# Performance work log

Measured on AMD Instinct MI355X. Metric: run time of the kernel, lower is better.

The kernel has to match this reference:

```python
import jax, jax.numpy as jnp
import numpy as np

N, D, B = 50000, 256, 2048
SIGMA = 1.0
SIGMA2 = SIGMA * SIGMA  # module stores np.square(sigma)


def setup_inputs() -> dict:
    key = jax.random.key(0)
    k1, k2, k3, k4 = jax.random.split(key, 4)
    x = jax.random.normal(k1, (B, D), dtype=jnp.float32)
    data_set = jax.random.normal(k2, (N, D), dtype=jnp.float32)
    # labels are +/-1
    data_labels = jnp.where(jax.random.uniform(k3, (N,)) < 0.5, -1.0, 1.0).astype(jnp.float32)
    # lambdas initialized to ones in the module; use small positive noise around 1/n scale
    lambdas = jax.random.uniform(k4, (N,), dtype=jnp.float32) * (2.0 / N)
    b = jnp.ones((1,), dtype=jnp.float32)
    return {"x": x, "data_set": data_set, "data_labels": data_labels,
            "lambdas": lambdas, "b": b}


def reference(x, data_set, data_labels, lambdas, b):
    x2 = jnp.sum(x * x, axis=1, keepdims=True)            # [B,1]
    s2 = jnp.sum(data_set * data_set, axis=1)             # [N]
    cross = jnp.einsum('bd,nd->bn', x, data_set)          # [B,N]
    sqdist = x2 + s2[None, :] - 2.0 * cross               # [B,N]
    K = jnp.exp(-sqdist / (2.0 * SIGMA2))                 # rbf kernel [B,N]
    w = data_labels * jax.nn.relu(lambdas)                # [N]
    return jnp.tanh(K @ w + b)                            # [B]
```

## Files before the change

### kernel.cpp

```cpp
#include <hip/hip_runtime.h>
#include <hip/hip_bf16.h>
#include <math.h>

#define NPTS 50000
#define DIM  256
#define BQ   2048
#define NPAD 50048

#define BK   32
#define CH   64
#define NCH  782
#define NG   48
#define LOG2E 1.4426950408889634f

#define WS_ACC 0
#define WS_X2  2048
#define WS_T   4096
#define WS_SGN 54144
#define WS_XB  104192
#define WS_SB  366336
#define WS_TOTAL_BYTES (6772480ull * 4ull)

#define V1_ACC 0
#define V1_X2  2048
#define V1_S2  4096
#define V1_W   54096

typedef __bf16 bf16x8 __attribute__((ext_vector_type(8)));
typedef __bf16 bf16x4 __attribute__((ext_vector_type(4)));
typedef float  f32x4  __attribute__((ext_vector_type(4)));
typedef unsigned int u32;

__device__ __forceinline__ float fast_exp2(float v) {
#if __has_builtin(__builtin_amdgcn_exp2f)
  return __builtin_amdgcn_exp2f(v);
#else
  return exp2f(v);
#endif
}

__device__ __forceinline__ void async_copy16(const __bf16* g, __bf16* l) {
  __builtin_amdgcn_global_load_lds(
      (const __attribute__((address_space(1))) u32*)g,
      (__attribute__((address_space(3))) u32*)l, 16, 0, 0);
}


__global__ __launch_bounds__(256) void svm_precvt9(
    const float* __restrict__ x, const float* __restrict__ s,
    const float* __restrict__ labels, const float* __restrict__ lambdas,
    float* __restrict__ ws) {
  const int wid  = blockIdx.x * 4 + (threadIdx.x >> 6);
  const int lane = threadIdx.x & 63;
  __bf16* xb = (__bf16*)(ws + WS_XB);
  __bf16* sb = (__bf16*)(ws + WS_SB);

  if (blockIdx.x < 8) ws[WS_ACC + blockIdx.x * 256 + threadIdx.x] = 0.0f;

  if (wid < NPAD) {
    float4 v = make_float4(0.f, 0.f, 0.f, 0.f);
    if (wid < NPTS)
      v = reinterpret_cast<const float4*>(s + (size_t)wid * DIM)[lane];
    bf16x4 h = { (__bf16)v.x, (__bf16)v.y, (__bf16)v.z, (__bf16)v.w };
    *reinterpret_cast<bf16x4*>(sb + (size_t)wid * DIM + lane * 4) = h;
    float ss = v.x * v.x + v.y * v.y + v.z * v.z + v.w * v.w;
    #pragma unroll
    for (int off = 32; off > 0; off >>= 1) ss += __shfl_xor(ss, off);
    if (lane == 0) {
      float s2h = 0.5f * LOG2E * ss;
      float lam = (wid < NPTS) ? lambdas[wid] : 0.0f;
      float lab = (wid < NPTS) ? labels[wid] : 1.0f;
      float mag = lam > 0.0f ? lam : 0.0f;
      ws[WS_T + wid]   = (mag > 0.0f) ? s2h - log2f(mag) : __builtin_inff();
      ws[WS_SGN + wid] = lab;
    }
  } else if (wid < NPAD + BQ) {
    int r = wid - NPAD;
    float4 v = reinterpret_cast<const float4*>(x + (size_t)r * DIM)[lane];
    bf16x4 h = { (__bf16)v.x, (__bf16)v.y, (__bf16)v.z, (__bf16)v.w };
    *reinterpret_cast<bf16x4*>(xb + (size_t)r * DIM + lane * 4) = h;
    float ss = v.x * v.x + v.y * v.y + v.z * v.z + v.w * v.w;
    #pragma unroll
    for (int off = 32; off > 0; off >>= 1) ss += __shfl_xor(ss, off);
    if (lane == 0) ws[WS_X2 + r] = 0.5f * LOG2E * ss;
  }
}

__global__ __launch_bounds__(256, 2) void svm_main9(float* __restrict__ ws) {
  __shared__ __bf16 sB[8 * CH * 32];

  const __bf16* xb = (const __bf16*)(ws + WS_XB);
  const __bf16* sb = (const __bf16*)(ws + WS_SB);
  const float* x2g = ws + WS_X2;
  const float* tg  = ws + WS_T;
  const float* sgg = ws + WS_SGN;
  float* accOut    = ws + WS_ACC;

  const int t    = threadIdx.x;
  const int wave = t >> 6;
  const int lane = t & 63;
  const int quad = lane >> 4;
  const int l16  = lane & 15;
  const int g    = blockIdx.x & 47;
  const int mt   = blockIdx.x / 48;
  const int m0   = mt * 128;
  const int c0   = (NCH * g) / NG;
  const int c1   = (NCH * (g + 1)) / NG;

  f32x4 afr[2][8];
  #pragma unroll
  for (int mi = 0; mi < 2; ++mi)
    #pragma unroll
    for (int kt = 0; kt < 8; ++kt)
      afr[mi][kt] = *reinterpret_cast<const f32x4*>(
          xb + (size_t)(m0 + wave * 32 + mi * 16 + l16) * DIM + kt * BK + quad * 8);
  #pragma unroll
  for (int mi = 0; mi < 2; ++mi)
    #pragma unroll
    for (int kt = 0; kt < 8; ++kt)
      asm volatile("" : "+v"(afr[mi][kt]));

  float runAcc[2][4] = {{0.f, 0.f, 0.f, 0.f}, {0.f, 0.f, 0.f, 0.f}};

  const int srcswz = ((lane & 3) ^ ((lane >> 3) & 3)) * 8;
  const int rdswz = (quad ^ ((l16 >> 1) & 3)) * 8;

  for (int c = c0; c < c1; ++c) {
    __syncthreads();

    #pragma unroll
    for (int i = 0; i < 8; ++i) {
      int ch = wave * 8 + i;
      int kt = ch >> 2;
      int nb = (ch & 3) * 16;
      const __bf16* src = sb + (size_t)(c * CH + nb + (lane >> 2)) * DIM
                             + kt * BK + srcswz;
      async_copy16(src, &sB[kt * (CH * 32) + nb * 32] + lane * 8);
    }
    __syncthreads();

    f32x4 acc[2][4];
    #pragma unroll
    for (int mi = 0; mi < 2; ++mi)
      #pragma unroll
      for (int ni = 0; ni < 4; ++ni)
        acc[mi][ni] = (f32x4)(0.0f);

    #pragma unroll
    for (int kt = 0; kt < 8; ++kt) {
      bf16x8 bfv[4];
      #pragma unroll
      for (int ni = 0; ni < 4; ++ni)
        bfv[ni] = *reinterpret_cast<const bf16x8*>(
            &sB[kt * (CH * 32) + (ni * 16 + l16) * 32 + rdswz]);
      #pragma unroll
      for (int mi = 0; mi < 2; ++mi)
        #pragma unroll
        for (int ni = 0; ni < 4; ++ni)
          acc[mi][ni] = __builtin_amdgcn_mfma_f32_16x16x32_bf16(
              __builtin_bit_cast(bf16x8, afr[mi][kt]), bfv[ni],
              acc[mi][ni], 0, 0, 0);
    }

    float tt[4], sg[4];
    #pragma unroll
    for (int ni = 0; ni < 4; ++ni) {
      int n = c * CH + ni * 16 + l16;
      tt[ni] = tg[n];
      sg[ni] = sgg[n];
    }
    #pragma unroll
    for (int mi = 0; mi < 2; ++mi)
      #pragma unroll
      for (int reg = 0; reg < 4; ++reg) {
        float p = runAcc[mi][reg];
        #pragma unroll
        for (int ni = 0; ni < 4; ++ni)
          p = __builtin_fmaf(sg[ni],
                fast_exp2(__builtin_fmaf(acc[mi][ni][reg], LOG2E, -tt[ni])), p);
        runAcc[mi][reg] = p;
      }
  }

  #pragma unroll
  for (int mi = 0; mi < 2; ++mi)
    #pragma unroll
    for (int reg = 0; reg < 4; ++reg) {
      float v = runAcc[mi][reg];
      v += __shfl_xor(v, 1);
      v += __shfl_xor(v, 2);
      v += __shfl_xor(v, 4);
      v += __shfl_xor(v, 8);
      if (l16 == 0) {
        int row = m0 + wave * 32 + mi * 16 + quad * 4 + reg;
        atomicAdd(&accOut[row], fast_exp2(-x2g[row]) * v);
      }
    }
}


__global__ __launch_bounds__(256) void svm_precompute(
    const float* __restrict__ x, const float* __restrict__ s,
    const float* __restrict__ labels, const float* __restrict__ lambdas,
    float* __restrict__ ws) {
  int wid  = blockIdx.x * 4 + (threadIdx.x >> 6);
  int lane = threadIdx.x & 63;
  const float* src;
  if (wid < NPTS)           src = s + (size_t)wid * DIM;
  else if (wid < NPTS + BQ) src = x + (size_t)(wid - NPTS) * DIM;
  else return;
  float4 v = reinterpret_cast<const float4*>(src)[lane];
  float ss = v.x * v.x + v.y * v.y + v.z * v.z + v.w * v.w;
  #pragma unroll
  for (int off = 32; off > 0; off >>= 1) ss += __shfl_xor(ss, off);
  if (lane == 0) {
    if (wid < NPTS) {
      ws[V1_S2 + wid] = ss;
      float lam = lambdas[wid];
      ws[V1_W + wid] = labels[wid] * (lam > 0.0f ? lam : 0.0f);
    } else {
      ws[V1_X2 + (wid - NPTS)] = ss;
    }
  }
}

__global__ __launch_bounds__(256) void svm_main(
    const float* __restrict__ x, const float* __restrict__ s,
    const float* __restrict__ ws) {
  __shared__ __bf16 sA[128 * BK];
  __shared__ __bf16 sB2[128 * BK];

  const int t    = threadIdx.x;
  const int wave = t >> 6;
  const int lane = t & 63;
  const int quad = lane >> 4;
  const int l16  = lane & 15;
  const int wm   = (wave & 1) * 64;
  const int wn   = (wave >> 1) * 64;
  const int bRow0 = blockIdx.y * 128;
  const int n0    = blockIdx.x * 128;

  f32x4 acc[4][4];
  #pragma unroll
  for (int i = 0; i < 4; ++i)
    #pragma unroll
    for (int j = 0; j < 4; ++j)
      acc[i][j] = (f32x4)(0.0f);

  for (int kt = 0; kt < DIM / BK; ++kt) {
    const int k0 = kt * BK;
    __syncthreads();
    #pragma unroll
    for (int i = 0; i < 4; ++i) {
      int slot = t + i * 256;
      int r  = slot >> 3;
      int c4 = slot & 7;
      float4 va = reinterpret_cast<const float4*>(
          x + (size_t)(bRow0 + r) * DIM + k0)[c4];
      bf16x4 ha = { (__bf16)va.x, (__bf16)va.y, (__bf16)va.z, (__bf16)va.w };
      *reinterpret_cast<bf16x4*>(&sA[r * BK + c4 * 4]) = ha;

      int nrow = n0 + r;
      float4 vb = make_float4(0.f, 0.f, 0.f, 0.f);
      if (nrow < NPTS)
        vb = reinterpret_cast<const float4*>(
            s + (size_t)nrow * DIM + k0)[c4];
      bf16x4 hb = { (__bf16)vb.x, (__bf16)vb.y, (__bf16)vb.z, (__bf16)vb.w };
      *reinterpret_cast<bf16x4*>(&sB2[r * BK + c4 * 4]) = hb;
    }
    __syncthreads();

    bf16x8 af[4], bfv[4];
    #pragma unroll
    for (int mi = 0; mi < 4; ++mi)
      af[mi] = *reinterpret_cast<const bf16x8*>(
          &sA[(wm + mi * 16 + l16) * BK + quad * 8]);
    #pragma unroll
    for (int ni = 0; ni < 4; ++ni)
      bfv[ni] = *reinterpret_cast<const bf16x8*>(
          &sB2[(wn + ni * 16 + l16) * BK + quad * 8]);
    #pragma unroll
    for (int mi = 0; mi < 4; ++mi)
      #pragma unroll
      for (int ni = 0; ni < 4; ++ni)
        acc[mi][ni] = __builtin_amdgcn_mfma_f32_16x16x32_bf16(
            af[mi], bfv[ni], acc[mi][ni], 0, 0, 0);
  }

  const float* x2g = ws + V1_X2;
  const float* s2g = ws + V1_S2;
  const float* wg  = ws + V1_W;
  float* accOut    = (float*)ws + V1_ACC;

  float s2v[4], wv[4];
  #pragma unroll
  for (int ni = 0; ni < 4; ++ni) {
    int n = n0 + wn + ni * 16 + l16;
    bool ok = n < NPTS;
    s2v[ni] = ok ? s2g[n] : 0.0f;
    wv[ni]  = ok ? wg[n]  : 0.0f;
  }
  #pragma unroll
  for (int mi = 0; mi < 4; ++mi) {
    const int mbase = wm + mi * 16 + quad * 4;
    #pragma unroll
    for (int reg = 0; reg < 4; ++reg) {
      float x2r = x2g[bRow0 + mbase + reg];
      float ps = 0.0f;
      #pragma unroll
      for (int ni = 0; ni < 4; ++ni) {
        float cc = acc[mi][ni][reg];
        ps += __expf(__builtin_fmaf(-0.5f, x2r + s2v[ni], cc)) * wv[ni];
      }
      ps += __shfl_xor(ps, 1);
      ps += __shfl_xor(ps, 2);
      ps += __shfl_xor(ps, 4);
      ps += __shfl_xor(ps, 8);
      if (l16 == 0) atomicAdd(&accOut[bRow0 + mbase + reg], ps);
    }
  }
}


__global__ __launch_bounds__(256) void svm_finalize(
    const float* __restrict__ ws, const float* __restrict__ bias,
    float* __restrict__ out) {
  int i = blockIdx.x * 256 + threadIdx.x;
  if (i < BQ) out[i] = tanhf(ws[i] + bias[0]);
}

extern "C" void kernel_launch(void* const* d_in, const int* in_sizes, int n_in,
                              void* d_out, int out_size, void* d_ws, size_t ws_size,
                              hipStream_t stream) {
  const float* x       = (const float*)d_in[0];
  const float* s       = (const float*)d_in[1];
  const float* labels  = (const float*)d_in[2];
  const float* lambdas = (const float*)d_in[3];
  const float* bias    = (const float*)d_in[4];
  float* out = (float*)d_out;
  float* ws  = (float*)d_ws;

  if (ws_size >= WS_TOTAL_BYTES) {
    svm_precvt9<<<(NPAD + BQ + 3) / 4, 256, 0, stream>>>(x, s, labels, lambdas, ws);
    svm_main9<<<16 * NG, 256, 0, stream>>>(ws);
  } else {
    hipMemsetAsync(ws, 0, BQ * sizeof(float), stream);
    svm_precompute<<<(NPTS + BQ + 3) / 4, 256, 0, stream>>>(x, s, labels, lambdas, ws);
    dim3 grid(391, BQ / 128);
    svm_main<<<grid, 256, 0, stream>>>(x, s, ws);
  }
  svm_finalize<<<BQ / 256, 256, 0, stream>>>(ws, bias, out);
}
```

Measured before the change: 157.8 us.

## Switch RBF distance GEMM from bf16 to fp8 MFMA with wider N tiles

The pre-conversion kernel now packs x and data_set into fp8 instead of bf16, and the main kernel computes the cross products with 16x16x32 fp8 MFMA. Each chunk now holds 128 data points, with a new XOR-swizzled LDS layout, and each wave accumulates 8 N sub-tiles. This halves the bytes streamed for the 50k×256 dataset and uses the higher fp8 matrix throughput. In exchange the dot products lose accuracy, which is only tolerable if the kernel values stay small, and the bf16 fast path is removed: targets without fp8 fall back to the slow path.

Result: slower. 533.6 us (+238.2%).

```diff
diff --git a/kernel.cpp b/kernel.cpp
--- a/kernel.cpp
+++ b/kernel.cpp
@@ -7,19 +7,25 @@
 #define BQ   2048
 #define NPAD 50048
 
-#define BK   32
-#define CH   64
-#define NCH  782
+#define CH   128
+#define NCH  391
 #define NG   48
 #define LOG2E 1.4426950408889634f
+
+#if __has_builtin(__builtin_amdgcn_mfma_f32_16x16x32_fp8_fp8) && \
+    __has_builtin(__builtin_amdgcn_cvt_pk_fp8_f32)
+#define HAVE_FP8 1
+#else
+#define HAVE_FP8 0
+#endif
 
 #define WS_ACC 0
 #define WS_X2  2048
 #define WS_T   4096
 #define WS_SGN 54144
-#define WS_XB  104192
-#define WS_SB  366336
-#define WS_TOTAL_BYTES (6772480ull * 4ull)
+#define WS_XB8 104192
+#define WS_SB8 235264
+#define WS_FP8_BYTES (3438336ull * 4ull)
 
 #define V1_ACC 0
 #define V1_X2  2048
@@ -29,6 +35,7 @@
 typedef __bf16 bf16x8 __attribute__((ext_vector_type(8)));
 typedef __bf16 bf16x4 __attribute__((ext_vector_type(4)));
 typedef float  f32x4  __attribute__((ext_vector_type(4)));
+typedef long   i64x2  __attribute__((ext_vector_type(2)));
 typedef unsigned int u32;
 
 __device__ __forceinline__ float fast_exp2(float v) {
@@ -39,21 +46,22 @@
 #endif
 }
 
-__device__ __forceinline__ void async_copy16(const __bf16* g, __bf16* l) {
+__device__ __forceinline__ void async_copy16(const void* g, void* l) {
   __builtin_amdgcn_global_load_lds(
       (const __attribute__((address_space(1))) u32*)g,
       (__attribute__((address_space(3))) u32*)l, 16, 0, 0);
 }
 
-
-__global__ __launch_bounds__(256) void svm_precvt9(
+#if HAVE_FP8
+
+__global__ __launch_bounds__(256) void svm_precvt10(
     const float* __restrict__ x, const float* __restrict__ s,
     const float* __restrict__ labels, const float* __restrict__ lambdas,
     float* __restrict__ ws) {
   const int wid  = blockIdx.x * 4 + (threadIdx.x >> 6);
   const int lane = threadIdx.x & 63;
-  __bf16* xb = (__bf16*)(ws + WS_XB);
-  __bf16* sb = (__bf16*)(ws + WS_SB);
+  int* xb8 = (int*)(ws + WS_XB8);
+  int* sb8 = (int*)(ws + WS_SB8);
 
   if (blockIdx.x < 8) ws[WS_ACC + blockIdx.x * 256 + threadIdx.x] = 0.0f;
 
@@ -61,8 +69,9 @@
     float4 v = make_float4(0.f, 0.f, 0.f, 0.f);
     if (wid < NPTS)
       v = reinterpret_cast<const float4*>(s + (size_t)wid * DIM)[lane];
-    bf16x4 h = { (__bf16)v.x, (__bf16)v.y, (__bf16)v.z, (__bf16)v.w };
-    *reinterpret_cast<bf16x4*>(sb + (size_t)wid * DIM + lane * 4) = h;
+    int pk = __builtin_amdgcn_cvt_pk_fp8_f32(v.x, v.y, 0, false);
+    pk     = __builtin_amdgcn_cvt_pk_fp8_f32(v.z, v.w, pk, true);
+    sb8[(size_t)wid * 64 + lane] = pk;
     float ss = v.x * v.x + v.y * v.y + v.z * v.z + v.w * v.w;
     #pragma unroll
     for (int off = 32; off > 0; off >>= 1) ss += __shfl_xor(ss, off);
@@ -77,8 +86,9 @@
   } else if (wid < NPAD + BQ) {
     int r = wid - NPAD;
     float4 v = reinterpret_cast<const float4*>(x + (size_t)r * DIM)[lane];
-    bf16x4 h = { (__bf16)v.x, (__bf16)v.y, (__bf16)v.z, (__bf16)v.w };
-    *reinterpret_cast<bf16x4*>(xb + (size_t)r * DIM + lane * 4) = h;
+    int pk = __builtin_amdgcn_cvt_pk_fp8_f32(v.x, v.y, 0, false);
+    pk     = __builtin_amdgcn_cvt_pk_fp8_f32(v.z, v.w, pk, true);
+    xb8[(size_t)r * 64 + lane] = pk;
     float ss = v.x * v.x + v.y * v.y + v.z * v.z + v.w * v.w;
     #pragma unroll
     for (int off = 32; off > 0; off >>= 1) ss += __shfl_xor(ss, off);
@@ -86,11 +96,11 @@
   }
 }
 
-__global__ __launch_bounds__(256, 2) void svm_main9(float* __restrict__ ws) {
-  __shared__ __bf16 sB[8 * CH * 32];
-
-  const __bf16* xb = (const __bf16*)(ws + WS_XB);
-  const __bf16* sb = (const __bf16*)(ws + WS_SB);
+__global__ __launch_bounds__(256, 2) void svm_main10(float* __restrict__ ws) {
+  __shared__ char sB[CH * 256];
+
+  const char* xb8 = (const char*)(ws + WS_XB8);
+  const char* sb8 = (const char*)(ws + WS_SB8);
   const float* x2g = ws + WS_X2;
   const float* tg  = ws + WS_T;
   const float* sgg = ws + WS_SGN;
@@ -101,70 +111,77 @@
   const int lane = t & 63;
   const int quad = lane >> 4;
   const int l16  = lane & 15;
-  const int g    = blockIdx.x & 47;
-  const int mt   = blockIdx.x / 48;
-  const int m0   = mt * 128;
+  const int g    = blockIdx.x % NG;
+  const int mt   = blockIdx.x / NG;
+  const int m0w  = mt * 128 + wave * 32;
   const int c0   = (NCH * g) / NG;
   const int c1   = (NCH * (g + 1)) / NG;
 
-  f32x4 afr[2][8];
+  f32x4 afr[2][4];
   #pragma unroll
   for (int mi = 0; mi < 2; ++mi)
     #pragma unroll
-    for (int kt = 0; kt < 8; ++kt)
-      afr[mi][kt] = *reinterpret_cast<const f32x4*>(
-          xb + (size_t)(m0 + wave * 32 + mi * 16 + l16) * DIM + kt * BK + quad * 8);
+    for (int kp = 0; kp < 4; ++kp)
+      afr[mi][kp] = *reinterpret_cast<const f32x4*>(
+          xb8 + (size_t)(m0w + mi * 16 + l16) * 256 + quad * 64 + kp * 16);
   #pragma unroll
   for (int mi = 0; mi < 2; ++mi)
     #pragma unroll
-    for (int kt = 0; kt < 8; ++kt)
-      asm volatile("" : "+v"(afr[mi][kt]));
+    for (int kp = 0; kp < 4; ++kp)
+      asm volatile("" : "+v"(afr[mi][kp]));
 
   float runAcc[2][4] = {{0.f, 0.f, 0.f, 0.f}, {0.f, 0.f, 0.f, 0.f}};
 
-  const int srcswz = ((lane & 3) ^ ((lane >> 3) & 3)) * 8;
-  const int rdswz = (quad ^ ((l16 >> 1) & 3)) * 8;
+  const int rowin = lane >> 4;
+  const int p     = lane & 15;
 
   for (int c = c0; c < c1; ++c) {
     __syncthreads();
 
     #pragma unroll
     for (int i = 0; i < 8; ++i) {
-      int ch = wave * 8 + i;
-      int kt = ch >> 2;
-      int nb = (ch & 3) * 16;
-      const __bf16* src = sb + (size_t)(c * CH + nb + (lane >> 2)) * DIM
-                             + kt * BK + srcswz;
-      async_copy16(src, &sB[kt * (CH * 32) + nb * 32] + lane * 8);
+      int j = wave * 8 + i;
+      int n15 = ((j & 3) * 4 + rowin) & 15;
+      const char* src = sb8 + (size_t)(c * CH + j * 4) * 256
+                            + rowin * 256 + ((p ^ n15) * 16);
+      async_copy16(src, sB + j * 1024 + lane * 16);
     }
     __syncthreads();
 
-    f32x4 acc[2][4];
+    f32x4 acc[2][8];
     #pragma unroll
     for (int mi = 0; mi < 2; ++mi)
       #pragma unroll
-      for (int ni = 0; ni < 4; ++ni)
+      for (int ni = 0; ni < 8; ++ni)
         acc[mi][ni] = (f32x4)(0.0f);
 
     #pragma unroll
-    for (int kt = 0; kt < 8; ++kt) {
-      bf16x8 bfv[4];
-      #pragma unroll
-      for (int ni = 0; ni < 4; ++ni)
-        bfv[ni] = *reinterpret_cast<const bf16x8*>(
-            &sB[kt * (CH * 32) + (ni * 16 + l16) * 32 + rdswz]);
-      #pragma unroll
-      for (int mi = 0; mi < 2; ++mi)
+    for (int kp = 0; kp < 4; ++kp) {
+      f32x4 bfp[8];
+      #pragma unroll
+      for (int ni = 0; ni < 8; ++ni) {
+        int n = ni * 16 + l16;
+        bfp[ni] = *reinterpret_cast<const f32x4*>(
+            sB + n * 256 + (((quad * 4 + kp) ^ l16) * 16));
+      }
+      #pragma unroll
+      for (int h = 0; h < 2; ++h) {
         #pragma unroll
-        for (int ni = 0; ni < 4; ++ni)
-          acc[mi][ni] = __builtin_amdgcn_mfma_f32_16x16x32_bf16(
-              __builtin_bit_cast(bf16x8, afr[mi][kt]), bfv[ni],
-              acc[mi][ni], 0, 0, 0);
-    }
-
-    float tt[4], sg[4];
-    #pragma unroll
-    for (int ni = 0; ni < 4; ++ni) {
+        for (int mi = 0; mi < 2; ++mi) {
+          long av = __builtin_bit_cast(i64x2, afr[mi][kp])[h];
+          #pragma unroll
+          for (int ni = 0; ni < 8; ++ni) {
+            long bv = __builtin_bit_cast(i64x2, bfp[ni])[h];
+            acc[mi][ni] = __builtin_amdgcn_mfma_f32_16x16x32_fp8_fp8(
+                av, bv, acc[mi][ni], 0, 0, 0);
+          }
+        }
+      }
+    }
+
+    float tt[8], sg[8];
+    #pragma unroll
+    for (int ni = 0; ni < 8; ++ni) {
       int n = c * CH + ni * 16 + l16;
       tt[ni] = tg[n];
       sg[ni] = sgg[n];
@@ -173,12 +190,13 @@
     for (int mi = 0; mi < 2; ++mi)
       #pragma unroll
       for (int reg = 0; reg < 4; ++reg) {
-        float p = runAcc[mi][reg];
+        float pacc = runAcc[mi][reg];
         #pragma unroll
-        for (int ni = 0; ni < 4; ++ni)
-          p = __builtin_fmaf(sg[ni],
-                fast_exp2(__builtin_fmaf(acc[mi][ni][reg], LOG2E, -tt[ni])), p);
-        runAcc[mi][reg] = p;
+        for (int ni = 0; ni < 8; ++ni)
+          pacc = __builtin_fmaf(sg[ni],
+                   fast_exp2(__builtin_fmaf(acc[mi][ni][reg], LOG2E, -tt[ni])),
+                   pacc);
+        runAcc[mi][reg] = pacc;
       }
   }
 
@@ -192,11 +210,12 @@
       v += __shfl_xor(v, 4);
       v += __shfl_xor(v, 8);
       if (l16 == 0) {
-        int row = m0 + wave * 32 + mi * 16 + quad * 4 + reg;
+        int row = m0w + mi * 16 + quad * 4 + reg;
         atomicAdd(&accOut[row], fast_exp2(-x2g[row]) * v);
       }
     }
 }
+#endif
 
 
 __global__ __launch_bounds__(256) void svm_precompute(
@@ -227,8 +246,8 @@
 __global__ __launch_bounds__(256) void svm_main(
     const float* __restrict__ x, const float* __restrict__ s,
     const float* __restrict__ ws) {
-  __shared__ __bf16 sA[128 * BK];
-  __shared__ __bf16 sB2[128 * BK];
+  __shared__ __bf16 sA[128 * 32];
+  __shared__ __bf16 sB2[128 * 32];
 
   const int t    = threadIdx.x;
   const int wave = t >> 6;
@@ -247,8 +266,8 @@
     for (int j = 0; j < 4; ++j)
       acc[i][j] = (f32x4)(0.0f);
 
-  for (int kt = 0; kt < DIM / BK; ++kt) {
-    const int k0 = kt * BK;
+  for (int kt = 0; kt < DIM / 32; ++kt) {
+    const int k0 = kt * 32;
     __syncthreads();
     #pragma unroll
     for (int i = 0; i < 4; ++i) {
@@ -258,7 +277,7 @@
       float4 va = reinterpret_cast<const float4*>(
           x + (size_t)(bRow0 + r) * DIM + k0)[c4];
       bf16x4 ha = { (__bf16)va.x, (__bf16)va.y, (__bf16)va.z, (__bf16)va.w };
-      *reinterpret_cast<bf16x4*>(&sA[r * BK + c4 * 4]) = ha;
+      *reinterpret_cast<bf16x4*>(&sA[r * 32 + c4 * 4]) = ha;
 
       int nrow = n0 + r;
       float4 vb = make_float4(0.f, 0.f, 0.f, 0.f);
@@ -266,7 +285,7 @@
         vb = reinterpret_cast<const float4*>(
             s + (size_t)nrow * DIM + k0)[c4];
       bf16x4 hb = { (__bf16)vb.x, (__bf16)vb.y, (__bf16)vb.z, (__bf16)vb.w };
-      *reinterpret_cast<bf16x4*>(&sB2[r * BK + c4 * 4]) = hb;
+      *reinterpret_cast<bf16x4*>(&sB2[r * 32 + c4 * 4]) = hb;
     }
     __syncthreads();
 
@@ -274,11 +293,11 @@
     #pragma unroll
     for (int mi = 0; mi < 4; ++mi)
       af[mi] = *reinterpret_cast<const bf16x8*>(
-          &sA[(wm + mi * 16 + l16) * BK + quad * 8]);
+          &sA[(wm + mi * 16 + l16) * 32 + quad * 8]);
     #pragma unroll
     for (int ni = 0; ni < 4; ++ni)
       bfv[ni] = *reinterpret_cast<const bf16x8*>(
-          &sB2[(wn + ni * 16 + l16) * BK + quad * 8]);
+          &sB2[(wn + ni * 16 + l16) * 32 + quad * 8]);
     #pragma unroll
     for (int mi = 0; mi < 4; ++mi)
       #pragma unroll
@@ -340,14 +359,17 @@
   float* out = (float*)d_out;
   float* ws  = (float*)d_ws;
 
-  if (ws_size >= WS_TOTAL_BYTES) {
-    svm_precvt9<<<(NPAD + BQ + 3) / 4, 256, 0, stream>>>(x, s, labels, lambdas, ws);
-    svm_main9<<<16 * NG, 256, 0, stream>>>(ws);
-  } else {
-    hipMemsetAsync(ws, 0, BQ * sizeof(float), stream);
-    svm_precompute<<<(NPTS + BQ + 3) / 4, 256, 0, stream>>>(x, s, labels, lambdas, ws);
-    dim3 grid(391, BQ / 128);
-    svm_main<<<grid, 256, 0, stream>>>(x, s, ws);
-  }
+#if HAVE_FP8
+  if (ws_size >= WS_FP8_BYTES) {
+    svm_precvt10<<<(NPAD + BQ + 3) / 4, 256, 0, stream>>>(x, s, labels, lambdas, ws);
+    svm_main10<<<16 * NG, 256, 0, stream>>>(ws);
+    svm_finalize<<<BQ / 256, 256, 0, stream>>>(ws, bias, out);
+    return;
+  }
+#endif
+  hipMemsetAsync(ws, 0, BQ * sizeof(float), stream);
+  svm_precompute<<<(NPTS + BQ + 3) / 4, 256, 0, stream>>>(x, s, labels, lambdas, ws);
+  dim3 grid(391, BQ / 128);
+  svm_main<<<grid, 256, 0, stream>>>(x, s, ws);
   svm_finalize<<<BQ / 256, 256, 0, stream>>>(ws, bias, out);
 }
```

## Double-buffer LDS staging of support tiles and interleave threshold/sign data

Applied to the files above, without the earlier changes.

Switches the main kernel to a two-stage LDS ping-pong: the next chunk's support-vector tile is issued with async global-to-LDS loads while MFMAs run on the current one, removing one barrier per iteration. The per-point threshold and label arrays are packed as float2 pairs and staged into LDS with the tile rather than read from global memory in the epilogue. The exp accumulation is split into two independent chains to shorten the dependency. LDS use doubles, which may affect the two-blocks-per-CU occupancy target.

Measured after the change: 174.4 us. +10.5%, slower.

```diff
diff --git a/kernel.cpp b/kernel.cpp
--- a/kernel.cpp
+++ b/kernel.cpp
@@ -13,10 +13,10 @@
 #define NG   48
 #define LOG2E 1.4426950408889634f
 
+
 #define WS_ACC 0
 #define WS_X2  2048
-#define WS_T   4096
-#define WS_SGN 54144
+#define WS_TSG 4096
 #define WS_XB  104192
 #define WS_SB  366336
 #define WS_TOTAL_BYTES (6772480ull * 4ull)
@@ -32,21 +32,17 @@
 typedef unsigned int u32;
 
 __device__ __forceinline__ float fast_exp2(float v) {
-#if __has_builtin(__builtin_amdgcn_exp2f)
   return __builtin_amdgcn_exp2f(v);
-#else
-  return exp2f(v);
-#endif
-}
-
-__device__ __forceinline__ void async_copy16(const __bf16* g, __bf16* l) {
+}
+
+__device__ __forceinline__ void async_copy16(const void* g, void* l) {
   __builtin_amdgcn_global_load_lds(
       (const __attribute__((address_space(1))) u32*)g,
       (__attribute__((address_space(3))) u32*)l, 16, 0, 0);
 }
 
 
-__global__ __launch_bounds__(256) void svm_precvt9(
+__global__ __launch_bounds__(256) void svm_precvt13(
     const float* __restrict__ x, const float* __restrict__ s,
     const float* __restrict__ labels, const float* __restrict__ lambdas,
     float* __restrict__ ws) {
@@ -71,8 +67,8 @@
       float lam = (wid < NPTS) ? lambdas[wid] : 0.0f;
       float lab = (wid < NPTS) ? labels[wid] : 1.0f;
       float mag = lam > 0.0f ? lam : 0.0f;
-      ws[WS_T + wid]   = (mag > 0.0f) ? s2h - log2f(mag) : __builtin_inff();
-      ws[WS_SGN + wid] = lab;
+      float tv  = (mag > 0.0f) ? s2h - log2f(mag) : __builtin_inff();
+      *reinterpret_cast<float2*>(&ws[WS_TSG + 2 * wid]) = make_float2(tv, lab);
     }
   } else if (wid < NPAD + BQ) {
     int r = wid - NPAD;
@@ -86,14 +82,14 @@
   }
 }
 
-__global__ __launch_bounds__(256, 2) void svm_main9(float* __restrict__ ws) {
-  __shared__ __bf16 sB[8 * CH * 32];
+__global__ __launch_bounds__(256, 2) void svm_main13(float* __restrict__ ws) {
+  __shared__ __bf16 sB[2][8 * CH * 32];
+  __shared__ float2 sTsg[2][CH];
 
   const __bf16* xb = (const __bf16*)(ws + WS_XB);
   const __bf16* sb = (const __bf16*)(ws + WS_SB);
+  const char* tsgb = (const char*)(ws + WS_TSG);
   const float* x2g = ws + WS_X2;
-  const float* tg  = ws + WS_T;
-  const float* sgg = ws + WS_SGN;
   float* accOut    = ws + WS_ACC;
 
   const int t    = threadIdx.x;
@@ -101,9 +97,9 @@
   const int lane = t & 63;
   const int quad = lane >> 4;
   const int l16  = lane & 15;
-  const int g    = blockIdx.x & 47;
-  const int mt   = blockIdx.x / 48;
-  const int m0   = mt * 128;
+  const int g    = blockIdx.x % NG;
+  const int mt   = blockIdx.x / NG;
+  const int m0w  = mt * 128 + wave * 32;
   const int c0   = (NCH * g) / NG;
   const int c1   = (NCH * (g + 1)) / NG;
 
@@ -113,7 +109,7 @@
     #pragma unroll
     for (int kt = 0; kt < 8; ++kt)
       afr[mi][kt] = *reinterpret_cast<const f32x4*>(
-          xb + (size_t)(m0 + wave * 32 + mi * 16 + l16) * DIM + kt * BK + quad * 8);
+          xb + (size_t)(m0w + mi * 16 + l16) * DIM + kt * BK + quad * 8);
   #pragma unroll
   for (int mi = 0; mi < 2; ++mi)
     #pragma unroll
@@ -123,11 +119,9 @@
   float runAcc[2][4] = {{0.f, 0.f, 0.f, 0.f}, {0.f, 0.f, 0.f, 0.f}};
 
   const int srcswz = ((lane & 3) ^ ((lane >> 3) & 3)) * 8;
-  const int rdswz = (quad ^ ((l16 >> 1) & 3)) * 8;
-
-  for (int c = c0; c < c1; ++c) {
-    __syncthreads();
-
+  const int rdswz  = (quad ^ ((l16 >> 1) & 3)) * 8;
+
+  auto stage = [&](int c, int b) {
     #pragma unroll
     for (int i = 0; i < 8; ++i) {
       int ch = wave * 8 + i;
@@ -135,9 +129,19 @@
       int nb = (ch & 3) * 16;
       const __bf16* src = sb + (size_t)(c * CH + nb + (lane >> 2)) * DIM
                              + kt * BK + srcswz;
-      async_copy16(src, &sB[kt * (CH * 32) + nb * 32] + lane * 8);
-    }
+      async_copy16(src, &sB[b][kt * (CH * 32) + nb * 32] + lane * 8);
+    }
+    if (lane < 8)
+      async_copy16(tsgb + (size_t)c * CH * 8 + wave * 128 + lane * 16,
+                   (char*)&sTsg[b][0] + wave * 128 + lane * 16);
+  };
+
+  stage(c0, 0);
+
+  for (int c = c0; c < c1; ++c) {
+    const int cur = (c - c0) & 1;
     __syncthreads();
+    if (c + 1 < c1) stage(c + 1, 1 - cur);
 
     f32x4 acc[2][4];
     #pragma unroll
@@ -152,7 +156,7 @@
       #pragma unroll
       for (int ni = 0; ni < 4; ++ni)
         bfv[ni] = *reinterpret_cast<const bf16x8*>(
-            &sB[kt * (CH * 32) + (ni * 16 + l16) * 32 + rdswz]);
+            &sB[cur][kt * (CH * 32) + (ni * 16 + l16) * 32 + rdswz]);
       #pragma unroll
       for (int mi = 0; mi < 2; ++mi)
         #pragma unroll
@@ -165,20 +169,23 @@
     float tt[4], sg[4];
     #pragma unroll
     for (int ni = 0; ni < 4; ++ni) {
-      int n = c * CH + ni * 16 + l16;
-      tt[ni] = tg[n];
-      sg[ni] = sgg[n];
+      float2 tsv = sTsg[cur][ni * 16 + l16];
+      tt[ni] = tsv.x;
+      sg[ni] = tsv.y;
     }
     #pragma unroll
     for (int mi = 0; mi < 2; ++mi)
       #pragma unroll
       for (int reg = 0; reg < 4; ++reg) {
-        float p = runAcc[mi][reg];
-        #pragma unroll
-        for (int ni = 0; ni < 4; ++ni)
-          p = __builtin_fmaf(sg[ni],
-                fast_exp2(__builtin_fmaf(acc[mi][ni][reg], LOG2E, -tt[ni])), p);
-        runAcc[mi][reg] = p;
+        float p0 = __builtin_fmaf(sg[0],
+            fast_exp2(__builtin_fmaf(acc[mi][0][reg], LOG2E, -tt[0])), 0.0f);
+        float p1 = __builtin_fmaf(sg[1],
+            fast_exp2(__builtin_fmaf(acc[mi][1][reg], LOG2E, -tt[1])), 0.0f);
+        p0 = __builtin_fmaf(sg[2],
+            fast_exp2(__builtin_fmaf(acc[mi][2][reg], LOG2E, -tt[2])), p0);
+        p1 = __builtin_fmaf(sg[3],
+            fast_exp2(__builtin_fmaf(acc[mi][3][reg], LOG2E, -tt[3])), p1);
+        runAcc[mi][reg] += p0 + p1;
       }
   }
 
@@ -192,7 +199,7 @@
       v += __shfl_xor(v, 4);
       v += __shfl_xor(v, 8);
       if (l16 == 0) {
-        int row = m0 + wave * 32 + mi * 16 + quad * 4 + reg;
+        int row = m0w + mi * 16 + quad * 4 + reg;
         atomicAdd(&accOut[row], fast_exp2(-x2g[row]) * v);
       }
     }
@@ -341,8 +348,8 @@
   float* ws  = (float*)d_ws;
 
   if (ws_size >= WS_TOTAL_BYTES) {
-    svm_precvt9<<<(NPAD + BQ + 3) / 4, 256, 0, stream>>>(x, s, labels, lambdas, ws);
-    svm_main9<<<16 * NG, 256, 0, stream>>>(ws);
+    svm_precvt13<<<(NPAD + BQ + 3) / 4, 256, 0, stream>>>(x, s, labels, lambdas, ws);
+    svm_main13<<<16 * NG, 256, 0, stream>>>(ws);
   } else {
     hipMemsetAsync(ws, 0, BQ * sizeof(float), stream);
     svm_precompute<<<(NPTS + BQ + 3) / 4, 256, 0, stream>>>(x, s, labels, lambdas, ws);
```
